# Performance work log

Measured on AMD Instinct MI355X. Metric: run time of the kernel, lower is better.

## Reference

```python
import jax, jax.numpy as jnp
import numpy as np

IN_F = 4096
OUT_F = 4096
NNZ = int(0.01 * IN_F * OUT_F)
ALPHA = 1.0


def setup_inputs() -> dict:
    key = jax.random.key(0)
    k1, k2, k3, k4, k5 = jax.random.split(key, 5)
    x = jax.random.normal(k1, (4, 2048, IN_F), dtype=jnp.float32)
    base_weights = (jax.random.normal(k2, (OUT_F, IN_F), dtype=jnp.float32) * 0.02).astype(jnp.float16)
    # sparse outlier correction in COO form (equivalent content to the CSR buffers)
    ortho_vals = (jax.random.normal(k3, (NNZ,), dtype=jnp.float32) * 1e-3).astype(jnp.float16)
    ortho_rows = jax.random.randint(k4, (NNZ,), 0, OUT_F, dtype=jnp.int32)
    ortho_cols = jax.random.randint(k5, (NNZ,), 0, IN_F, dtype=jnp.int32)
    return {"x": x, "base_weights": base_weights, "ortho_vals": ortho_vals,
            "ortho_rows": ortho_rows, "ortho_cols": ortho_cols}


def reference(x, base_weights, ortho_vals, ortho_rows, ortho_cols):
    orig_shape = x.shape
    orig_dtype = x.dtype
    x_flat = x.reshape(-1, IN_F)  # [N, in]

    # Base stream: fp16 GEMM, then cast to fp32 (matches torch.mm on fp16)
    out_base = jnp.matmul(x_flat.astype(jnp.float16), base_weights.T).astype(jnp.float32)

    # Ortho stream: sparse (out,in) correction applied in fp32.
    # Scatter the sparse values into a dense fp32 matrix once (cheap: 64MB),
    # then use a dense GEMM — same math as torch.sparse.mm(W_csr, x^T)^T.
    w_ortho = jnp.zeros((OUT_F, IN_F), dtype=jnp.float32).at[ortho_rows, ortho_cols].add(
        ortho_vals.astype(jnp.float32))
    out_ortho = jnp.matmul(x_flat.astype(jnp.float32), w_ortho.T)  # [N, out]

    out_flat = out_base + ALPHA * out_ortho
    return out_flat.reshape(orig_shape[:-1] + (OUT_F,)).astype(orig_dtype)
```

## Files before the change

kernel.cpp:

```cpp
#include <hip/hip_runtime.h>

typedef _Float16 f16;
typedef unsigned short u16;
typedef unsigned int u32;
typedef long long i64;
typedef __attribute__((ext_vector_type(8))) _Float16 f16x8;
typedef __attribute__((ext_vector_type(4))) float f32x4;

#define IN_F 4096
#define OUT_F 4096

__device__ __forceinline__ void gload16(const f16* g, f16* l) {
  __builtin_amdgcn_global_load_lds(
      (const __attribute__((address_space(1))) void*)g,
      (__attribute__((address_space(3))) void*)l, 16, 0, 0);
}

__global__ __launch_bounds__(256) void cvt_f32_f16(
    const float* __restrict__ in, f16* __restrict__ out, i64 n8) {
  i64 s = (i64)gridDim.x * blockDim.x;
  for (i64 j = (i64)blockIdx.x * blockDim.x + threadIdx.x; j < n8; j += s) {
    float4 a = ((const float4*)in)[2 * j];
    float4 b = ((const float4*)in)[2 * j + 1];
    f16x8 o;
    o[0] = (f16)a.x; o[1] = (f16)a.y; o[2] = (f16)a.z; o[3] = (f16)a.w;
    o[4] = (f16)b.x; o[5] = (f16)b.y; o[6] = (f16)b.z; o[7] = (f16)b.w;
    ((f16x8*)out)[j] = o;
  }
}

__global__ __launch_bounds__(256) void zero32(u32* __restrict__ p, i64 n) {
  i64 s = (i64)gridDim.x * blockDim.x;
  for (i64 j = (i64)blockIdx.x * blockDim.x + threadIdx.x; j < n; j += s) p[j] = 0u;
}

__global__ __launch_bounds__(256) void scatter_woh(
    const float* __restrict__ vals, const int* __restrict__ rows,
    const int* __restrict__ cols, f16* __restrict__ woh, int nnz) {
  int i = blockIdx.x * blockDim.x + threadIdx.x;
  if (i >= nnz) return;
  int r = rows[i], c = cols[i];
  if (r < 0 || r >= OUT_F || c < 0 || c >= IN_F) return;
  float v = vals[i];
  size_t idx = (size_t)r * IN_F + c;
  u32* p = (u32*)woh + (idx >> 1);
  u32 sh = (u32)(idx & 1) * 16u;
  union { f16 h; u16 u; } cv;
  u32 old = *p;
  while (true) {
    u32 assumed = old;
    cv.u = (u16)((assumed >> sh) & 0xFFFFu);
    float cur = (float)cv.h;
    cv.h = (f16)(cur + v);
    u32 nw = (assumed & ~(0xFFFFu << sh)) | ((u32)cv.u << sh);
    old = atomicCAS(p, assumed, nw);
    if (old == assumed) break;
  }
}

template <int STREAM>
__global__ __launch_bounds__(512, 2) void gemm_256(
    const f16* __restrict__ Xh, const f16* __restrict__ Bm,
    float* __restrict__ out, int M) {
  __shared__ alignas(16) f16 As[2][16384];
  __shared__ alignas(16) f16 Bs[2][16384];

  const int tid = threadIdx.x;
  const int lane = tid & 63;
  const int wave = tid >> 6;
  const int wr = wave >> 2;
  const int wc = wave & 3;
  const int lo = lane & 15, hi = lane >> 4, l7 = lane & 7;

  const int bid = (int)blockIdx.x;
  const int nbn = OUT_F / 256;
  const int nwg = (M / 256) * nbn;
  const int swz = ((nwg & 7) == 0) ? ((bid & 7) * (nwg >> 3) + (bid >> 3)) : bid;
  const int brow = (swz / nbn) << 8;
  const int bcol = (swz % nbn) << 8;

  int aglob[4], bglob[4], ldst[4];
#pragma unroll
  for (int i = 0; i < 4; ++i) {
    int c = i * 512 + tid;
    int row = c >> 3;
    int kc = (c & 7) ^ (row & 7);
    ldst[i] = c * 8;
    aglob[i] = (brow + row) * IN_F + kc * 8;
    bglob[i] = (bcol + row) * IN_F + kc * 8;
  }

  const int abase = (wr * 128 + lo) * 64;
  const int bbase = (wc * 64 + lo) * 64;
  const int slot0 = ((hi) ^ l7) * 8;
  const int slot1 = ((4 + hi) ^ l7) * 8;

  f32x4 acc[8][4] = {};

#pragma unroll
  for (int i = 0; i < 4; ++i) gload16(Xh + aglob[i], &As[0][ldst[i]]);
#pragma unroll
  for (int i = 0; i < 4; ++i) gload16(Bm + bglob[i], &Bs[0][ldst[i]]);
  asm volatile("s_waitcnt vmcnt(0)" ::: "memory");
  __builtin_amdgcn_sched_barrier(0);
  __builtin_amdgcn_s_barrier();

  const int NT = IN_F / 64;
  for (int kt = 0; kt < NT; ++kt) {
    const f16* A = As[kt & 1];
    const f16* B = Bs[kt & 1];
    f16* An = (f16*)As[(kt & 1) ^ 1];
    f16* Bn = (f16*)Bs[(kt & 1) ^ 1];
    const int kn = (kt + 1) * 64;
    const bool pf = (kt + 1 < NT);

    f16x8 bf[4][2];
    f16x8 af[2][2];

#pragma unroll
    for (int nf = 0; nf < 4; ++nf) {
      bf[nf][0] = *(const f16x8*)(B + bbase + nf * 1024 + slot0);
      bf[nf][1] = *(const f16x8*)(B + bbase + nf * 1024 + slot1);
    }
    af[0][0] = *(const f16x8*)(A + abase + 0 * 1024 + slot0);
    af[0][1] = *(const f16x8*)(A + abase + 0 * 1024 + slot1);
    af[1][0] = *(const f16x8*)(A + abase + 1 * 1024 + slot0);
    af[1][1] = *(const f16x8*)(A + abase + 1 * 1024 + slot1);
    if (pf) { gload16(Xh + aglob[0] + kn, An + ldst[0]);
              gload16(Xh + aglob[1] + kn, An + ldst[1]); }
    __builtin_amdgcn_s_barrier();
    __builtin_amdgcn_s_setprio(1);
#pragma unroll
    for (int mm = 0; mm < 2; ++mm)
#pragma unroll
      for (int nf = 0; nf < 4; ++nf) {
        acc[mm][nf] = __builtin_amdgcn_mfma_f32_16x16x32_f16(af[mm][0], bf[nf][0], acc[mm][nf], 0, 0, 0);
        acc[mm][nf] = __builtin_amdgcn_mfma_f32_16x16x32_f16(af[mm][1], bf[nf][1], acc[mm][nf], 0, 0, 0);
      }
    __builtin_amdgcn_s_setprio(0);
    __builtin_amdgcn_s_barrier();

    af[0][0] = *(const f16x8*)(A + abase + 2 * 1024 + slot0);
    af[0][1] = *(const f16x8*)(A + abase + 2 * 1024 + slot1);
    af[1][0] = *(const f16x8*)(A + abase + 3 * 1024 + slot0);
    af[1][1] = *(const f16x8*)(A + abase + 3 * 1024 + slot1);
    if (pf) { gload16(Xh + aglob[2] + kn, An + ldst[2]);
              gload16(Xh + aglob[3] + kn, An + ldst[3]); }
    __builtin_amdgcn_s_barrier();
    __builtin_amdgcn_s_setprio(1);
#pragma unroll
    for (int mm = 0; mm < 2; ++mm)
#pragma unroll
      for (int nf = 0; nf < 4; ++nf) {
        acc[2 + mm][nf] = __builtin_amdgcn_mfma_f32_16x16x32_f16(af[mm][0], bf[nf][0], acc[2 + mm][nf], 0, 0, 0);
        acc[2 + mm][nf] = __builtin_amdgcn_mfma_f32_16x16x32_f16(af[mm][1], bf[nf][1], acc[2 + mm][nf], 0, 0, 0);
      }
    __builtin_amdgcn_s_setprio(0);
    __builtin_amdgcn_s_barrier();

    af[0][0] = *(const f16x8*)(A + abase + 4 * 1024 + slot0);
    af[0][1] = *(const f16x8*)(A + abase + 4 * 1024 + slot1);
    af[1][0] = *(const f16x8*)(A + abase + 5 * 1024 + slot0);
    af[1][1] = *(const f16x8*)(A + abase + 5 * 1024 + slot1);
    if (pf) { gload16(Bm + bglob[0] + kn, Bn + ldst[0]);
              gload16(Bm + bglob[1] + kn, Bn + ldst[1]); }
    __builtin_amdgcn_s_barrier();
    __builtin_amdgcn_s_setprio(1);
#pragma unroll
    for (int mm = 0; mm < 2; ++mm)
#pragma unroll
      for (int nf = 0; nf < 4; ++nf) {
        acc[4 + mm][nf] = __builtin_amdgcn_mfma_f32_16x16x32_f16(af[mm][0], bf[nf][0], acc[4 + mm][nf], 0, 0, 0);
        acc[4 + mm][nf] = __builtin_amdgcn_mfma_f32_16x16x32_f16(af[mm][1], bf[nf][1], acc[4 + mm][nf], 0, 0, 0);
      }
    __builtin_amdgcn_s_setprio(0);
    __builtin_amdgcn_s_barrier();

    af[0][0] = *(const f16x8*)(A + abase + 6 * 1024 + slot0);
    af[0][1] = *(const f16x8*)(A + abase + 6 * 1024 + slot1);
    af[1][0] = *(const f16x8*)(A + abase + 7 * 1024 + slot0);
    af[1][1] = *(const f16x8*)(A + abase + 7 * 1024 + slot1);
    if (pf) { gload16(Bm + bglob[2] + kn, Bn + ldst[2]);
              gload16(Bm + bglob[3] + kn, Bn + ldst[3]); }
    __builtin_amdgcn_s_barrier();
    __builtin_amdgcn_s_setprio(1);
#pragma unroll
    for (int mm = 0; mm < 2; ++mm)
#pragma unroll
      for (int nf = 0; nf < 4; ++nf) {
        acc[6 + mm][nf] = __builtin_amdgcn_mfma_f32_16x16x32_f16(af[mm][0], bf[nf][0], acc[6 + mm][nf], 0, 0, 0);
        acc[6 + mm][nf] = __builtin_amdgcn_mfma_f32_16x16x32_f16(af[mm][1], bf[nf][1], acc[6 + mm][nf], 0, 0, 0);
      }
    __builtin_amdgcn_s_setprio(0);

    if (pf) {
      asm volatile("s_waitcnt vmcnt(0)" ::: "memory");
      __builtin_amdgcn_sched_barrier(0);
    }
    __builtin_amdgcn_s_barrier();
  }

  const int crow0 = brow + wr * 128 + (hi << 2);
  const int ccol0 = bcol + wc * 64 + lo;
#pragma unroll
  for (int mf = 0; mf < 8; ++mf)
#pragma unroll
    for (int nf = 0; nf < 4; ++nf)
#pragma unroll
      for (int r = 0; r < 4; ++r) {
        float* p = out + (size_t)(crow0 + mf * 16 + r) * OUT_F + (ccol0 + nf * 16);
        if constexpr (STREAM == 0)
          *p = (float)(f16)acc[mf][nf][r];
        else
          *p += acc[mf][nf][r];
      }
}

template <bool A16, int STREAM>
__global__ __launch_bounds__(256, 2) void gemm_one(
    const float* __restrict__ Xf, const f16* __restrict__ Xh,
    const f16* __restrict__ Bm, float* __restrict__ out, int M) {
  constexpr int LDA = A16 ? 32 : 40;
  __shared__ alignas(16) f16 As[128 * LDA];
  __shared__ alignas(16) f16 Bs[128 * 32];

  const int tid = threadIdx.x, lane = tid & 63, wave = tid >> 6;
  const int wr = wave >> 1, wc = wave & 1;
  const int nbn = OUT_F / 128;
  const int nwg = (int)gridDim.x;
  const int bid = (int)blockIdx.x;
  const int swz = ((nwg & 7) == 0) ? ((bid & 7) * (nwg >> 3) + (bid >> 3)) : bid;
  const int brow = (swz / nbn) << 7;
  const int bcol = (swz % nbn) << 7;

  f32x4 acc[4][4] = {};
  const int srow = tid >> 2, sk = (tid & 3) * 8;
  const f16* gB = Bm + (size_t)(bcol + srow) * IN_F + sk;
  f16* sB = Bs + tid * 8;
  const f16*   gA = A16 ? (Xh + (size_t)(brow + srow) * IN_F + sk) : (const f16*)nullptr;
  const float* gX = A16 ? (const float*)nullptr : (Xf + (size_t)(brow + srow) * IN_F + sk);
  f16* sA  = As + tid * 8;
  f16* sAr = As + srow * LDA + sk;
  const f16* pa = As + (wr * 64 + (lane & 15)) * LDA + (lane >> 4) * 8;
  const f16* pb = Bs + (wc * 64 + (lane & 15)) * 32 + (lane >> 4) * 8;

  for (int k0 = 0; k0 < IN_F; k0 += 32) {
    if constexpr (A16) {
      gload16(gA + k0, sA);
      gload16(gA + k0 + (size_t)64 * IN_F, sA + 2048);
    } else {
      float4 u0 = *(const float4*)(gX + k0);
      float4 u1 = *(const float4*)(gX + k0 + 4);
      float4 v0 = *(const float4*)(gX + k0 + (size_t)64 * IN_F);
      float4 v1 = *(const float4*)(gX + k0 + (size_t)64 * IN_F + 4);
      f16x8 h0, h1;
      h0[0] = (f16)u0.x; h0[1] = (f16)u0.y; h0[2] = (f16)u0.z; h0[3] = (f16)u0.w;
      h0[4] = (f16)u1.x; h0[5] = (f16)u1.y; h0[6] = (f16)u1.z; h0[7] = (f16)u1.w;
      h1[0] = (f16)v0.x; h1[1] = (f16)v0.y; h1[2] = (f16)v0.z; h1[3] = (f16)v0.w;
      h1[4] = (f16)v1.x; h1[5] = (f16)v1.y; h1[6] = (f16)v1.z; h1[7] = (f16)v1.w;
      *(f16x8*)sAr = h0;
      *(f16x8*)(sAr + 64 * LDA) = h1;
    }
    gload16(gB + k0, sB);
    gload16(gB + k0 + (size_t)64 * IN_F, sB + 2048);
    __syncthreads();
    f16x8 af[4], bfr[4];
#pragma unroll
    for (int m = 0; m < 4; ++m) af[m] = *(const f16x8*)(pa + m * 16 * LDA);
#pragma unroll
    for (int n = 0; n < 4; ++n) bfr[n] = *(const f16x8*)(pb + n * 512);
#pragma unroll
    for (int m = 0; m < 4; ++m)
#pragma unroll
      for (int n = 0; n < 4; ++n)
        acc[m][n] = __builtin_amdgcn_mfma_f32_16x16x32_f16(af[m], bfr[n], acc[m][n], 0, 0, 0);
    __syncthreads();
  }
  const int crow0 = brow + wr * 64 + ((lane >> 4) << 2);
  const int ccol0 = bcol + wc * 64 + (lane & 15);
#pragma unroll
  for (int m = 0; m < 4; ++m)
#pragma unroll
    for (int n = 0; n < 4; ++n)
#pragma unroll
      for (int r = 0; r < 4; ++r) {
        float* p = out + (size_t)(crow0 + m * 16 + r) * OUT_F + (ccol0 + n * 16);
        if constexpr (STREAM == 0) *p = (float)(f16)acc[m][n][r];
        else *p += acc[m][n][r];
      }
}

extern "C" void kernel_launch(void* const* d_in, const int* in_sizes, int n_in,
                              void* d_out, int out_size, void* d_ws, size_t ws_size,
                              hipStream_t stream) {
  const float* x    = (const float*)d_in[0];
  const float* W    = (const float*)d_in[1];
  const float* vals = (const float*)d_in[2];
  const int*   rows = (const int*)d_in[3];
  const int*   cols = (const int*)d_in[4];
  float*       out  = (float*)d_out;

  const i64 total_x = (i64)in_sizes[0];
  const int M   = (int)(total_x / IN_F);
  const int nnz = in_sizes[2];
  if (M <= 0 || M % 128 != 0) return;

  const size_t whb = (size_t)OUT_F * IN_F * 2;
  const size_t xhb = (size_t)M * IN_F * 2;

  if (ws_size >= xhb + 2 * whb) {
    f16* xh  = (f16*)d_ws;
    f16* wh  = (f16*)((char*)d_ws + xhb);
    f16* woh = (f16*)((char*)d_ws + xhb + whb);
    cvt_f32_f16<<<2048, 256, 0, stream>>>(x, xh, total_x / 8);
    cvt_f32_f16<<<2048, 256, 0, stream>>>(W, wh, (i64)OUT_F * IN_F / 8);
    zero32<<<2048, 256, 0, stream>>>((u32*)woh, (i64)(whb / 4));
    scatter_woh<<<(nnz + 255) / 256, 256, 0, stream>>>(vals, rows, cols, woh, nnz);
    if (M % 256 == 0) {
      const int grid = (M / 256) * (OUT_F / 256);
      gemm_256<0><<<grid, 512, 0, stream>>>(xh, wh, out, M);
      gemm_256<1><<<grid, 512, 0, stream>>>(xh, woh, out, M);
    } else {
      const int grid = (M / 128) * (OUT_F / 128);
      gemm_one<true, 0><<<grid, 256, 0, stream>>>(nullptr, xh, wh, out, M);
      gemm_one<true, 1><<<grid, 256, 0, stream>>>(nullptr, xh, woh, out, M);
    }
  } else if (ws_size >= 2 * whb) {
    f16* wh  = (f16*)d_ws;
    f16* woh = (f16*)((char*)d_ws + whb);
    cvt_f32_f16<<<2048, 256, 0, stream>>>(W, wh, (i64)OUT_F * IN_F / 8);
    zero32<<<2048, 256, 0, stream>>>((u32*)woh, (i64)(whb / 4));
    scatter_woh<<<(nnz + 255) / 256, 256, 0, stream>>>(vals, rows, cols, woh, nnz);
    const int grid = (M / 128) * (OUT_F / 128);
    gemm_one<false, 0><<<grid, 256, 0, stream>>>(x, nullptr, wh, out, M);
    gemm_one<false, 1><<<grid, 256, 0, stream>>>(x, nullptr, woh, out, M);
  }
}
```

Before: 656.9 us.

## Use 1024-thread blocks for the 256x256 GEMM tile with 16 waves

The 256x256 GEMM now launches 1024-thread blocks (16 waves in a 4x4 grid), so each wave computes a 64x64 sub-tile instead of 128x64. Per-wave accumulators are halved and the global-to-LDS loads are spread over more threads. The aim is more waves per CU to hide latency. The cost is more waves contending for each barrier and less register-level reuse of the B fragments, which could lower MFMA efficiency.

```diff
diff --git a/kernel.cpp b/kernel.cpp
--- a/kernel.cpp
+++ b/kernel.cpp
@@ -59,7 +59,7 @@
 }
 
 template <int STREAM>
-__global__ __launch_bounds__(512, 2) void gemm_256(
+__global__ __launch_bounds__(1024, 4) void gemm_1k(
     const f16* __restrict__ Xh, const f16* __restrict__ Bm,
     float* __restrict__ out, int M) {
   __shared__ alignas(16) f16 As[2][16384];
@@ -79,28 +79,24 @@
   const int brow = (swz / nbn) << 8;
   const int bcol = (swz % nbn) << 8;
 
-  int aglob[4], bglob[4], ldst[4];
-#pragma unroll
-  for (int i = 0; i < 4; ++i) {
-    int c = i * 512 + tid;
-    int row = c >> 3;
-    int kc = (c & 7) ^ (row & 7);
-    ldst[i] = c * 8;
-    aglob[i] = (brow + row) * IN_F + kc * 8;
-    bglob[i] = (bcol + row) * IN_F + kc * 8;
-  }
-
-  const int abase = (wr * 128 + lo) * 64;
+  const int row0 = tid >> 3;
+  const int kc0  = (tid & 7) ^ (row0 & 7);
+  const int ldst = tid * 8;
+  const i64 ag = (i64)(brow + row0) * IN_F + kc0 * 8;
+  const i64 bg = (i64)(bcol + row0) * IN_F + kc0 * 8;
+  const i64 hstep = (i64)128 * IN_F;
+
+  const int abase = (wr * 64 + lo) * 64;
   const int bbase = (wc * 64 + lo) * 64;
-  const int slot0 = ((hi) ^ l7) * 8;
+  const int slot0 = (hi ^ l7) * 8;
   const int slot1 = ((4 + hi) ^ l7) * 8;
 
-  f32x4 acc[8][4] = {};
-
-#pragma unroll
-  for (int i = 0; i < 4; ++i) gload16(Xh + aglob[i], &As[0][ldst[i]]);
-#pragma unroll
-  for (int i = 0; i < 4; ++i) gload16(Bm + bglob[i], &Bs[0][ldst[i]]);
+  f32x4 acc[4][4] = {};
+
+  gload16(Xh + ag, &As[0][ldst]);
+  gload16(Bm + bg, &Bs[0][ldst]);
+  gload16(Xh + ag + hstep, &As[0][ldst + 8192]);
+  gload16(Bm + bg + hstep, &Bs[0][ldst + 8192]);
   asm volatile("s_waitcnt vmcnt(0)" ::: "memory");
   __builtin_amdgcn_sched_barrier(0);
   __builtin_amdgcn_s_barrier();
@@ -114,85 +110,63 @@
     const int kn = (kt + 1) * 64;
     const bool pf = (kt + 1 < NT);
 
-    f16x8 bf[4][2];
-    f16x8 af[2][2];
+    f16x8 bf[4][2], af[2];
 
 #pragma unroll
     for (int nf = 0; nf < 4; ++nf) {
       bf[nf][0] = *(const f16x8*)(B + bbase + nf * 1024 + slot0);
       bf[nf][1] = *(const f16x8*)(B + bbase + nf * 1024 + slot1);
     }
-    af[0][0] = *(const f16x8*)(A + abase + 0 * 1024 + slot0);
-    af[0][1] = *(const f16x8*)(A + abase + 0 * 1024 + slot1);
-    af[1][0] = *(const f16x8*)(A + abase + 1 * 1024 + slot0);
-    af[1][1] = *(const f16x8*)(A + abase + 1 * 1024 + slot1);
-    if (pf) { gload16(Xh + aglob[0] + kn, An + ldst[0]);
-              gload16(Xh + aglob[1] + kn, An + ldst[1]); }
+    af[0] = *(const f16x8*)(A + abase + 0 * 1024 + slot0);
+    af[1] = *(const f16x8*)(A + abase + 0 * 1024 + slot1);
+    if (pf) { gload16(Xh + ag + kn, An + ldst);
+              gload16(Bm + bg + kn, Bn + ldst); }
     __builtin_amdgcn_s_barrier();
     __builtin_amdgcn_s_setprio(1);
 #pragma unroll
-    for (int mm = 0; mm < 2; ++mm)
-#pragma unroll
-      for (int nf = 0; nf < 4; ++nf) {
-        acc[mm][nf] = __builtin_amdgcn_mfma_f32_16x16x32_f16(af[mm][0], bf[nf][0], acc[mm][nf], 0, 0, 0);
-        acc[mm][nf] = __builtin_amdgcn_mfma_f32_16x16x32_f16(af[mm][1], bf[nf][1], acc[mm][nf], 0, 0, 0);
-      }
+    for (int nf = 0; nf < 4; ++nf) {
+      acc[0][nf] = __builtin_amdgcn_mfma_f32_16x16x32_f16(af[0], bf[nf][0], acc[0][nf], 0, 0, 0);
+      acc[0][nf] = __builtin_amdgcn_mfma_f32_16x16x32_f16(af[1], bf[nf][1], acc[0][nf], 0, 0, 0);
+    }
     __builtin_amdgcn_s_setprio(0);
     __builtin_amdgcn_s_barrier();
 
-    af[0][0] = *(const f16x8*)(A + abase + 2 * 1024 + slot0);
-    af[0][1] = *(const f16x8*)(A + abase + 2 * 1024 + slot1);
-    af[1][0] = *(const f16x8*)(A + abase + 3 * 1024 + slot0);
-    af[1][1] = *(const f16x8*)(A + abase + 3 * 1024 + slot1);
-    if (pf) { gload16(Xh + aglob[2] + kn, An + ldst[2]);
-              gload16(Xh + aglob[3] + kn, An + ldst[3]); }
+    af[0] = *(const f16x8*)(A + abase + 1 * 1024 + slot0);
+    af[1] = *(const f16x8*)(A + abase + 1 * 1024 + slot1);
+    if (pf) { gload16(Xh + ag + hstep + kn, An + ldst + 8192);
+              gload16(Bm + bg + hstep + kn, Bn + ldst + 8192); }
     __builtin_amdgcn_s_barrier();
     __builtin_amdgcn_s_setprio(1);
 #pragma unroll
-    for (int mm = 0; mm < 2; ++mm)
-#pragma unroll
-      for (int nf = 0; nf < 4; ++nf) {
-        acc[2 + mm][nf] = __builtin_amdgcn_mfma_f32_16x16x32_f16(af[mm][0], bf[nf][0], acc[2 + mm][nf], 0, 0, 0);
-        acc[2 + mm][nf] = __builtin_amdgcn_mfma_f32_16x16x32_f16(af[mm][1], bf[nf][1], acc[2 + mm][nf], 0, 0, 0);
-      }
+    for (int nf = 0; nf < 4; ++nf) {
+      acc[1][nf] = __builtin_amdgcn_mfma_f32_16x16x32_f16(af[0], bf[nf][0], acc[1][nf], 0, 0, 0);
+      acc[1][nf] = __builtin_amdgcn_mfma_f32_16x16x32_f16(af[1], bf[nf][1], acc[1][nf], 0, 0, 0);
+    }
     __builtin_amdgcn_s_setprio(0);
     __builtin_amdgcn_s_barrier();
 
-    af[0][0] = *(const f16x8*)(A + abase + 4 * 1024 + slot0);
-    af[0][1] = *(const f16x8*)(A + abase + 4 * 1024 + slot1);
-    af[1][0] = *(const f16x8*)(A + abase + 5 * 1024 + slot0);
-    af[1][1] = *(const f16x8*)(A + abase + 5 * 1024 + slot1);
-    if (pf) { gload16(Bm + bglob[0] + kn, Bn + ldst[0]);
-              gload16(Bm + bglob[1] + kn, Bn + ldst[1]); }
+    af[0] = *(const f16x8*)(A + abase + 2 * 1024 + slot0);
+    af[1] = *(const f16x8*)(A + abase + 2 * 1024 + slot1);
     __builtin_amdgcn_s_barrier();
     __builtin_amdgcn_s_setprio(1);
 #pragma unroll
-    for (int mm = 0; mm < 2; ++mm)
-#pragma unroll
-      for (int nf = 0; nf < 4; ++nf) {
-        acc[4 + mm][nf] = __builtin_amdgcn_mfma_f32_16x16x32_f16(af[mm][0], bf[nf][0], acc[4 + mm][nf], 0, 0, 0);
-        acc[4 + mm][nf] = __builtin_amdgcn_mfma_f32_16x16x32_f16(af[mm][1], bf[nf][1], acc[4 + mm][nf], 0, 0, 0);
-      }
+    for (int nf = 0; nf < 4; ++nf) {
+      acc[2][nf] = __builtin_amdgcn_mfma_f32_16x16x32_f16(af[0], bf[nf][0], acc[2][nf], 0, 0, 0);
+      acc[2][nf] = __builtin_amdgcn_mfma_f32_16x16x32_f16(af[1], bf[nf][1], acc[2][nf], 0, 0, 0);
+    }
     __builtin_amdgcn_s_setprio(0);
     __builtin_amdgcn_s_barrier();
 
-    af[0][0] = *(const f16x8*)(A + abase + 6 * 1024 + slot0);
-    af[0][1] = *(const f16x8*)(A + abase + 6 * 1024 + slot1);
-    af[1][0] = *(const f16x8*)(A + abase + 7 * 1024 + slot0);
-    af[1][1] = *(const f16x8*)(A + abase + 7 * 1024 + slot1);
-    if (pf) { gload16(Bm + bglob[2] + kn, Bn + ldst[2]);
-              gload16(Bm + bglob[3] + kn, Bn + ldst[3]); }
+    af[0] = *(const f16x8*)(A + abase + 3 * 1024 + slot0);
+    af[1] = *(const f16x8*)(A + abase + 3 * 1024 + slot1);
     __builtin_amdgcn_s_barrier();
     __builtin_amdgcn_s_setprio(1);
 #pragma unroll
-    for (int mm = 0; mm < 2; ++mm)
-#pragma unroll
-      for (int nf = 0; nf < 4; ++nf) {
-        acc[6 + mm][nf] = __builtin_amdgcn_mfma_f32_16x16x32_f16(af[mm][0], bf[nf][0], acc[6 + mm][nf], 0, 0, 0);
-        acc[6 + mm][nf] = __builtin_amdgcn_mfma_f32_16x16x32_f16(af[mm][1], bf[nf][1], acc[6 + mm][nf], 0, 0, 0);
-      }
+    for (int nf = 0; nf < 4; ++nf) {
+      acc[3][nf] = __builtin_amdgcn_mfma_f32_16x16x32_f16(af[0], bf[nf][0], acc[3][nf], 0, 0, 0);
+      acc[3][nf] = __builtin_amdgcn_mfma_f32_16x16x32_f16(af[1], bf[nf][1], acc[3][nf], 0, 0, 0);
+    }
     __builtin_amdgcn_s_setprio(0);
-
     if (pf) {
       asm volatile("s_waitcnt vmcnt(0)" ::: "memory");
       __builtin_amdgcn_sched_barrier(0);
@@ -200,10 +174,10 @@
     __builtin_amdgcn_s_barrier();
   }
 
-  const int crow0 = brow + wr * 128 + (hi << 2);
+  const int crow0 = brow + wr * 64 + (hi << 2);
   const int ccol0 = bcol + wc * 64 + lo;
 #pragma unroll
-  for (int mf = 0; mf < 8; ++mf)
+  for (int mf = 0; mf < 4; ++mf)
 #pragma unroll
     for (int nf = 0; nf < 4; ++nf)
 #pragma unroll
@@ -318,8 +292,8 @@
     scatter_woh<<<(nnz + 255) / 256, 256, 0, stream>>>(vals, rows, cols, woh, nnz);
     if (M % 256 == 0) {
       const int grid = (M / 256) * (OUT_F / 256);
-      gemm_256<0><<<grid, 512, 0, stream>>>(xh, wh, out, M);
-      gemm_256<1><<<grid, 512, 0, stream>>>(xh, woh, out, M);
+      gemm_1k<0><<<grid, 1024, 0, stream>>>(xh, wh, out, M);
+      gemm_1k<1><<<grid, 1024, 0, stream>>>(xh, woh, out, M);
     } else {
       const int grid = (M / 128) * (OUT_F / 128);
       gemm_one<true, 0><<<grid, 256, 0, stream>>>(nullptr, xh, wh, out, M);
```

Result: no change. 649.0 us (-1.2%).

## Prefetch two K-tiles ahead and drop intra-iteration barriers in GEMM loop

Applied to the files above, without the earlier changes.

The GEMM main loop now issues global-to-LDS loads for tile kt+2 after finishing compute on tile kt, reusing the same buffer. It waits with vmcnt(8) so one tile's loads stay in flight across an iteration, instead of interleaving loads with four barrier-separated MFMA phases. This removes three of the four barriers per iteration and gives each load a full iteration of latency to hide. The cost is that the single remaining barrier must also guard buffer reuse, and the vmcnt accounting depends on each thread issuing exactly eight loads per tile. The MFMA work can no longer overlap with the loads for its own stage.

```diff
diff --git a/kernel.cpp b/kernel.cpp
--- a/kernel.cpp
+++ b/kernel.cpp
@@ -98,10 +98,16 @@
   f32x4 acc[8][4] = {};
 
 #pragma unroll
-  for (int i = 0; i < 4; ++i) gload16(Xh + aglob[i], &As[0][ldst[i]]);
-#pragma unroll
-  for (int i = 0; i < 4; ++i) gload16(Bm + bglob[i], &Bs[0][ldst[i]]);
-  asm volatile("s_waitcnt vmcnt(0)" ::: "memory");
+  for (int i = 0; i < 4; ++i) {
+    gload16(Xh + aglob[i], &As[0][ldst[i]]);
+    gload16(Bm + bglob[i], &Bs[0][ldst[i]]);
+  }
+#pragma unroll
+  for (int i = 0; i < 4; ++i) {
+    gload16(Xh + aglob[i] + 64, &As[1][ldst[i]]);
+    gload16(Bm + bglob[i] + 64, &Bs[1][ldst[i]]);
+  }
+  asm volatile("s_waitcnt vmcnt(8)" ::: "memory");
   __builtin_amdgcn_sched_barrier(0);
   __builtin_amdgcn_s_barrier();
 
@@ -109,95 +115,47 @@
   for (int kt = 0; kt < NT; ++kt) {
     const f16* A = As[kt & 1];
     const f16* B = Bs[kt & 1];
-    f16* An = (f16*)As[(kt & 1) ^ 1];
-    f16* Bn = (f16*)Bs[(kt & 1) ^ 1];
-    const int kn = (kt + 1) * 64;
-    const bool pf = (kt + 1 < NT);
 
     f16x8 bf[4][2];
-    f16x8 af[2][2];
-
 #pragma unroll
     for (int nf = 0; nf < 4; ++nf) {
       bf[nf][0] = *(const f16x8*)(B + bbase + nf * 1024 + slot0);
       bf[nf][1] = *(const f16x8*)(B + bbase + nf * 1024 + slot1);
     }
-    af[0][0] = *(const f16x8*)(A + abase + 0 * 1024 + slot0);
-    af[0][1] = *(const f16x8*)(A + abase + 0 * 1024 + slot1);
-    af[1][0] = *(const f16x8*)(A + abase + 1 * 1024 + slot0);
-    af[1][1] = *(const f16x8*)(A + abase + 1 * 1024 + slot1);
-    if (pf) { gload16(Xh + aglob[0] + kn, An + ldst[0]);
-              gload16(Xh + aglob[1] + kn, An + ldst[1]); }
+#pragma unroll
+    for (int q = 0; q < 4; ++q) {
+      f16x8 a00 = *(const f16x8*)(A + abase + (2 * q)     * 1024 + slot0);
+      f16x8 a01 = *(const f16x8*)(A + abase + (2 * q)     * 1024 + slot1);
+      f16x8 a10 = *(const f16x8*)(A + abase + (2 * q + 1) * 1024 + slot0);
+      f16x8 a11 = *(const f16x8*)(A + abase + (2 * q + 1) * 1024 + slot1);
+      __builtin_amdgcn_s_setprio(1);
+#pragma unroll
+      for (int nf = 0; nf < 4; ++nf) {
+        acc[2 * q][nf]     = __builtin_amdgcn_mfma_f32_16x16x32_f16(a00, bf[nf][0], acc[2 * q][nf], 0, 0, 0);
+        acc[2 * q][nf]     = __builtin_amdgcn_mfma_f32_16x16x32_f16(a01, bf[nf][1], acc[2 * q][nf], 0, 0, 0);
+        acc[2 * q + 1][nf] = __builtin_amdgcn_mfma_f32_16x16x32_f16(a10, bf[nf][0], acc[2 * q + 1][nf], 0, 0, 0);
+        acc[2 * q + 1][nf] = __builtin_amdgcn_mfma_f32_16x16x32_f16(a11, bf[nf][1], acc[2 * q + 1][nf], 0, 0, 0);
+      }
+      __builtin_amdgcn_s_setprio(0);
+    }
+
     __builtin_amdgcn_s_barrier();
-    __builtin_amdgcn_s_setprio(1);
-#pragma unroll
-    for (int mm = 0; mm < 2; ++mm)
-#pragma unroll
-      for (int nf = 0; nf < 4; ++nf) {
-        acc[mm][nf] = __builtin_amdgcn_mfma_f32_16x16x32_f16(af[mm][0], bf[nf][0], acc[mm][nf], 0, 0, 0);
-        acc[mm][nf] = __builtin_amdgcn_mfma_f32_16x16x32_f16(af[mm][1], bf[nf][1], acc[mm][nf], 0, 0, 0);
-      }
-    __builtin_amdgcn_s_setprio(0);
-    __builtin_amdgcn_s_barrier();
-
-    af[0][0] = *(const f16x8*)(A + abase + 2 * 1024 + slot0);
-    af[0][1] = *(const f16x8*)(A + abase + 2 * 1024 + slot1);
-    af[1][0] = *(const f16x8*)(A + abase + 3 * 1024 + slot0);
-    af[1][1] = *(const f16x8*)(A + abase + 3 * 1024 + slot1);
-    if (pf) { gload16(Xh + aglob[2] + kn, An + ldst[2]);
-              gload16(Xh + aglob[3] + kn, An + ldst[3]); }
-    __builtin_amdgcn_s_barrier();
-    __builtin_amdgcn_s_setprio(1);
-#pragma unroll
-    for (int mm = 0; mm < 2; ++mm)
-#pragma unroll
-      for (int nf = 0; nf < 4; ++nf) {
-        acc[2 + mm][nf] = __builtin_amdgcn_mfma_f32_16x16x32_f16(af[mm][0], bf[nf][0], acc[2 + mm][nf], 0, 0, 0);
-        acc[2 + mm][nf] = __builtin_amdgcn_mfma_f32_16x16x32_f16(af[mm][1], bf[nf][1], acc[2 + mm][nf], 0, 0, 0);
-      }
-    __builtin_amdgcn_s_setprio(0);
-    __builtin_amdgcn_s_barrier();
-
-    af[0][0] = *(const f16x8*)(A + abase + 4 * 1024 + slot0);
-    af[0][1] = *(const f16x8*)(A + abase + 4 * 1024 + slot1);
-    af[1][0] = *(const f16x8*)(A + abase + 5 * 1024 + slot0);
-    af[1][1] = *(const f16x8*)(A + abase + 5 * 1024 + slot1);
-    if (pf) { gload16(Bm + bglob[0] + kn, Bn + ldst[0]);
-              gload16(Bm + bglob[1] + kn, Bn + ldst[1]); }
-    __builtin_amdgcn_s_barrier();
-    __builtin_amdgcn_s_setprio(1);
-#pragma unroll
-    for (int mm = 0; mm < 2; ++mm)
-#pragma unroll
-      for (int nf = 0; nf < 4; ++nf) {
-        acc[4 + mm][nf] = __builtin_amdgcn_mfma_f32_16x16x32_f16(af[mm][0], bf[nf][0], acc[4 + mm][nf], 0, 0, 0);
-        acc[4 + mm][nf] = __builtin_amdgcn_mfma_f32_16x16x32_f16(af[mm][1], bf[nf][1], acc[4 + mm][nf], 0, 0, 0);
-      }
-    __builtin_amdgcn_s_setprio(0);
-    __builtin_amdgcn_s_barrier();
-
-    af[0][0] = *(const f16x8*)(A + abase + 6 * 1024 + slot0);
-    af[0][1] = *(const f16x8*)(A + abase + 6 * 1024 + slot1);
-    af[1][0] = *(const f16x8*)(A + abase + 7 * 1024 + slot0);
-    af[1][1] = *(const f16x8*)(A + abase + 7 * 1024 + slot1);
-    if (pf) { gload16(Bm + bglob[2] + kn, Bn + ldst[2]);
-              gload16(Bm + bglob[3] + kn, Bn + ldst[3]); }
-    __builtin_amdgcn_s_barrier();
-    __builtin_amdgcn_s_setprio(1);
-#pragma unroll
-    for (int mm = 0; mm < 2; ++mm)
-#pragma unroll
-      for (int nf = 0; nf < 4; ++nf) {
-        acc[6 + mm][nf] = __builtin_amdgcn_mfma_f32_16x16x32_f16(af[mm][0], bf[nf][0], acc[6 + mm][nf], 0, 0, 0);
-        acc[6 + mm][nf] = __builtin_amdgcn_mfma_f32_16x16x32_f16(af[mm][1], bf[nf][1], acc[6 + mm][nf], 0, 0, 0);
-      }
-    __builtin_amdgcn_s_setprio(0);
-
-    if (pf) {
-      asm volatile("s_waitcnt vmcnt(0)" ::: "memory");
+    if (kt + 2 < NT) {
+      f16* An = (f16*)As[kt & 1];
+      f16* Bn = (f16*)Bs[kt & 1];
+      const int kn = (kt + 2) * 64;
+#pragma unroll
+      for (int i = 0; i < 4; ++i) {
+        gload16(Xh + aglob[i] + kn, An + ldst[i]);
+        gload16(Bm + bglob[i] + kn, Bn + ldst[i]);
+      }
+    }
+    if (kt + 1 < NT) {
+      if (kt + 2 < NT) asm volatile("s_waitcnt vmcnt(8)" ::: "memory");
+      else             asm volatile("s_waitcnt vmcnt(0)" ::: "memory");
       __builtin_amdgcn_sched_barrier(0);
-    }
-    __builtin_amdgcn_s_barrier();
+      __builtin_amdgcn_s_barrier();
+    }
   }
 
   const int crow0 = brow + wr * 128 + (hi << 2);
```

New measurement: 623.0 us. 1.05x faster.
